# Optimization experiments

Measured on AMD Instinct MI355X. Metric: run time of the kernel, lower is better.

## Reference

```python
import jax, jax.numpy as jnp
import numpy as np

RADIUS = 12
SIGMA = 5.0
USM_LO, USM_HI = 0.0, 5.0
BEGIN = 0  # cfg.usm_begin_param


def _gauss_kernel_2d():
    x = jnp.arange(-RADIUS, RADIUS + 1, dtype=jnp.float32)
    k = jnp.exp(-0.5 * (x / SIGMA) ** 2)
    k = k / k.sum()
    return jnp.outer(k, k)  # [25, 25]


def setup_inputs() -> dict:
    key = jax.random.key(0)
    k1, k2 = jax.random.split(key)
    img = jax.random.uniform(k1, (16, 3, 512, 512), dtype=jnp.float32)
    features = jax.random.normal(k2, (16, 8), dtype=jnp.float32)
    return {"img": img, "features": features}


def reference(img, features):
    p = features[:, BEGIN:BEGIN + 1]                       # [B, 1]
    param = (jnp.tanh(p) * 0.5 + 0.5) * (USM_HI - USM_LO) + USM_LO

    # depthwise 25x25 gaussian blur with reflect padding
    kernel = jnp.broadcast_to(_gauss_kernel_2d(), (3, 1, 25, 25))  # OIHW, groups=3
    padded = jnp.pad(img, ((0, 0), (0, 0), (RADIUS, RADIUS), (RADIUS, RADIUS)),
                     mode='reflect')
    blurred = jax.lax.conv_general_dilated(
        padded, kernel, window_strides=(1, 1), padding='VALID',
        dimension_numbers=('NCHW', 'OIHW', 'NCHW'), feature_group_count=3)

    out = img + param.reshape(-1, 1, 1, 1) * (img - blurred)
    return out, param
```

## Files before the change

### kernel.cpp

```cpp
#include <hip/hip_runtime.h>
#include <hip/hip_fp16.h>


#define RADIUS 12
#define KS     25
#define TILE   64
#define PT     (TILE + 2 * RADIUS)
#define TA_LD  104
#define TB_LD  72
#define IMG_W  512
#define IMG_H  512
#define PLANE  (IMG_W * IMG_H)
#define NPLANE 48

__device__ __constant__ float GW[KS] = {
    0.00453456f, 0.00718308f, 0.01093238f, 0.01598625f, 0.02245983f,
    0.03031760f, 0.03931982f, 0.04899550f, 0.05865827f, 0.06747307f,
    0.07456928f, 0.07918039f, 0.08077993f, 0.07918039f, 0.07456928f,
    0.06747307f, 0.05865827f, 0.04899550f, 0.03931982f, 0.03031760f,
    0.02245983f, 0.01598625f, 0.01093238f, 0.00718308f, 0.00453456f
};

__device__ __forceinline__ int reflect512(int i) {
    i = (i < 0) ? -i : i;
    return (i >= 512) ? (1022 - i) : i;
}

typedef _Float16 h2_t __attribute__((ext_vector_type(2)));

__device__ __forceinline__ unsigned h2u(__half2 h) {
    union { __half2 h; unsigned u; } x; x.h = h; return x.u;
}
__device__ __forceinline__ float u_lo(unsigned u) {
    union { unsigned u; __half2 h; } x; x.u = u;
    return __half2float(__low2half(x.h));
}
__device__ __forceinline__ float u_hi(unsigned u) {
    union { unsigned u; __half2 h; } x; x.u = u;
    return __half2float(__high2half(x.h));
}

#if __has_builtin(__builtin_amdgcn_fdot2)
#define HAVE_DOT2 1
__device__ __forceinline__ float fdot2u(unsigned a, unsigned b, float c) {
    union { unsigned u; h2_t h; } ua, ub;
    ua.u = a; ub.u = b;
    return __builtin_amdgcn_fdot2(ua.h, ub.h, c, false);
}
#else
#define HAVE_DOT2 0
__device__ __forceinline__ float fdot2u(unsigned a, unsigned b, float c) {
    return c + u_lo(a) * u_lo(b) + u_hi(a) * u_hi(b);
}
#endif

__global__ __launch_bounds__(256) void usm_fused_kernel(
    const float* __restrict__ img, const float* __restrict__ feat,
    float* __restrict__ out, float* __restrict__ out_param)
{
    __shared__ __half tileA[PT][TA_LD];
    __shared__ __half tmpB[PT][TB_LD];

    const int tid = threadIdx.x;
    const int tx0 = blockIdx.x * TILE, ty0 = blockIdx.y * TILE;
    const int zc = blockIdx.z, b = zc / 3;
    const float param = (tanhf(feat[b * 8]) * 0.5f + 0.5f) * 5.0f;
    const float* __restrict__ src = img + (size_t)zc * PLANE;
    const bool xedge = (blockIdx.x == 0) || (blockIdx.x == 7);

    unsigned W2[12];
#pragma unroll
    for (int m = 0; m < 12; ++m)
        W2[m] = h2u(__floats2half2_rn(GW[2 * m], GW[2 * m + 1]));
    const unsigned WE = h2u(__floats2half2_rn(GW[24], 0.f));
    const unsigned WO = h2u(__floats2half2_rn(0.f, GW[24]));

    for (int li = tid; li < PT * 11; li += 256) {
        int py = li / 11, s = li - py * 11;
        int gy = reflect512(ty0 - RADIUS + py);
        const float* rowp = src + gy * IMG_W;
        int gx = tx0 - RADIUS + s * 8;
        float4 va, vb;
        if (!xedge) {
            va = *(const float4*)(rowp + gx);
            vb = *(const float4*)(rowp + gx + 4);
        } else {
            va.x = rowp[reflect512(gx)];     va.y = rowp[reflect512(gx + 1)];
            va.z = rowp[reflect512(gx + 2)]; va.w = rowp[reflect512(gx + 3)];
            vb.x = rowp[reflect512(gx + 4)]; vb.y = rowp[reflect512(gx + 5)];
            vb.z = rowp[reflect512(gx + 6)]; vb.w = rowp[reflect512(gx + 7)];
        }
        uint4 pk;
        pk.x = h2u(__floats2half2_rn(va.x, va.y));
        pk.y = h2u(__floats2half2_rn(va.z, va.w));
        pk.z = h2u(__floats2half2_rn(vb.x, vb.y));
        pk.w = h2u(__floats2half2_rn(vb.z, vb.w));
        *(uint4*)&tileA[py][s * 8] = pk;
    }
    __syncthreads();

    for (int li = tid; li < PT * (TILE / 8); li += 256) {
        const int py = li >> 3, g = li & 7;
        const uint4 qa = *(const uint4*)&tileA[py][g * 8];
        const uint4 qb = *(const uint4*)&tileA[py][g * 8 + 8];
        const uint4 qc = *(const uint4*)&tileA[py][g * 8 + 16];
        const uint4 qd = *(const uint4*)&tileA[py][g * 8 + 24];

        unsigned P[16] = { qa.x, qa.y, qa.z, qa.w, qb.x, qb.y, qb.z, qb.w,
                           qc.x, qc.y, qc.z, qc.w, qd.x, qd.y, qd.z, qd.w };
        unsigned S[15];
#pragma unroll
        for (int i = 0; i < 15; ++i)
            S[i] = __builtin_amdgcn_alignbit(P[i + 1], P[i], 16);

        float acc[8];
#pragma unroll
        for (int h = 0; h < 4; ++h) {
            float a = 0.f;
#pragma unroll
            for (int m = 0; m < 12; ++m) a = fdot2u(P[h + m], W2[m], a);
            acc[2 * h] = fdot2u(P[h + 12], WE, a);
        }
#pragma unroll
        for (int h = 0; h < 4; ++h) {
            float a = 0.f;
#pragma unroll
            for (int m = 0; m < 12; ++m) a = fdot2u(S[h + m], W2[m], a);
            acc[2 * h + 1] = fdot2u(P[h + 12], WO, a);
        }

        uint4 pk;
        pk.x = h2u(__floats2half2_rn(acc[0], acc[1]));
        pk.y = h2u(__floats2half2_rn(acc[2], acc[3]));
        pk.z = h2u(__floats2half2_rn(acc[4], acc[5]));
        pk.w = h2u(__floats2half2_rn(acc[6], acc[7]));
        *(uint4*)&tmpB[py][g * 8] = pk;
    }
    __syncthreads();

    const int tx4 = (tid & 15) * 4, ry0 = (tid >> 4) * 4;
    float ax[4], ay[4], az[4], aw[4];
#pragma unroll
    for (int d = 0; d < 4; ++d) ax[d] = ay[d] = az[d] = aw[d] = 0.f;

#pragma unroll
    for (int k = 0; k < KS + 3; ++k) {
        uint2 rd = *(const uint2*)&tmpB[ry0 + k][tx4];
        const float c0 = u_lo(rd.x), c1 = u_hi(rd.x);
        const float c2 = u_lo(rd.y), c3 = u_hi(rd.y);
#pragma unroll
        for (int d = 0; d < 4; ++d) {
            int kk = k - d;
            if (kk >= 0 && kk < KS) {
                const float wk = GW[kk];
                ax[d] += wk * c0; ay[d] += wk * c1;
                az[d] += wk * c2; aw[d] += wk * c3;
            }
        }
    }

    float* __restrict__ dst = out + (size_t)zc * PLANE;
#pragma unroll
    for (int d = 0; d < 4; ++d) {
        const int oy = ty0 + ry0 + d;
        float4 v = *(const float4*)(src + (size_t)oy * IMG_W + tx0 + tx4);
        float4 o;
        o.x = v.x + param * (v.x - ax[d]);
        o.y = v.y + param * (v.y - ay[d]);
        o.z = v.z + param * (v.z - az[d]);
        o.w = v.w + param * (v.w - aw[d]);
        *(float4*)(dst + (size_t)oy * IMG_W + tx0 + tx4) = o;
    }

    if (tid == 0 && blockIdx.x == 0 && blockIdx.y == 0 && (zc - b * 3) == 0)
        out_param[b] = param;
}

extern "C" void kernel_launch(void* const* d_in, const int* in_sizes, int n_in,
                              void* d_out, int out_size, void* d_ws, size_t ws_size,
                              hipStream_t stream) {
    const float* img  = (const float*)d_in[0];
    const float* feat = (const float*)d_in[1];
    float* out       = (float*)d_out;
    float* out_param = (float*)d_out + (size_t)NPLANE * PLANE;

    usm_fused_kernel<<<dim3(8, 8, NPLANE), 256, 0, stream>>>(img, feat, out, out_param);
}
```

Measured before the change: 42.17 us.

## Swizzle block order, unroll staging loops, use fp16 vertical FMA and LDS center

Result: faster. 40.44 us (-4.1%).

```diff
diff --git a/kernel.cpp b/kernel.cpp
--- a/kernel.cpp
+++ b/kernel.cpp
@@ -13,6 +13,9 @@
 #define PLANE  (IMG_W * IMG_H)
 #define NPLANE 48
 
+#define N_STAGE (PT * 11)
+#define N_H     (PT * (TILE / 8))
+
 __device__ __constant__ float GW[KS] = {
     0.00453456f, 0.00718308f, 0.01093238f, 0.01598625f, 0.02245983f,
     0.03031760f, 0.03931982f, 0.04899550f, 0.05865827f, 0.06747307f,
@@ -31,24 +34,23 @@
 __device__ __forceinline__ unsigned h2u(__half2 h) {
     union { __half2 h; unsigned u; } x; x.h = h; return x.u;
 }
+__device__ __forceinline__ __half2 u2h(unsigned u) {
+    union { unsigned u; __half2 h; } x; x.u = u; return x.h;
+}
 __device__ __forceinline__ float u_lo(unsigned u) {
-    union { unsigned u; __half2 h; } x; x.u = u;
-    return __half2float(__low2half(x.h));
+    return __half2float(__low2half(u2h(u)));
 }
 __device__ __forceinline__ float u_hi(unsigned u) {
-    union { unsigned u; __half2 h; } x; x.u = u;
-    return __half2float(__high2half(x.h));
+    return __half2float(__high2half(u2h(u)));
 }
 
 #if __has_builtin(__builtin_amdgcn_fdot2)
-#define HAVE_DOT2 1
 __device__ __forceinline__ float fdot2u(unsigned a, unsigned b, float c) {
     union { unsigned u; h2_t h; } ua, ub;
     ua.u = a; ub.u = b;
     return __builtin_amdgcn_fdot2(ua.h, ub.h, c, false);
 }
 #else
-#define HAVE_DOT2 0
 __device__ __forceinline__ float fdot2u(unsigned a, unsigned b, float c) {
     return c + u_lo(a) * u_lo(b) + u_hi(a) * u_hi(b);
 }
@@ -61,12 +63,18 @@
     __shared__ __half tileA[PT][TA_LD];
     __shared__ __half tmpB[PT][TB_LD];
 
+    const int bid  = blockIdx.x + 8 * blockIdx.y + 64 * blockIdx.z;
+    const int swz  = (bid & 7) * 384 + (bid >> 3);
+    const int bx   = swz & 7;
+    const int by   = (swz >> 3) & 7;
+    const int zc   = swz >> 6;
+
     const int tid = threadIdx.x;
-    const int tx0 = blockIdx.x * TILE, ty0 = blockIdx.y * TILE;
-    const int zc = blockIdx.z, b = zc / 3;
+    const int tx0 = bx * TILE, ty0 = by * TILE;
+    const int b   = zc / 3;
     const float param = (tanhf(feat[b * 8]) * 0.5f + 0.5f) * 5.0f;
     const float* __restrict__ src = img + (size_t)zc * PLANE;
-    const bool xedge = (blockIdx.x == 0) || (blockIdx.x == 7);
+    const bool xedge = (bx == 0) || (bx == 7);
 
     unsigned W2[12];
 #pragma unroll
@@ -75,86 +83,98 @@
     const unsigned WE = h2u(__floats2half2_rn(GW[24], 0.f));
     const unsigned WO = h2u(__floats2half2_rn(0.f, GW[24]));
 
-    for (int li = tid; li < PT * 11; li += 256) {
-        int py = li / 11, s = li - py * 11;
-        int gy = reflect512(ty0 - RADIUS + py);
-        const float* rowp = src + gy * IMG_W;
-        int gx = tx0 - RADIUS + s * 8;
-        float4 va, vb;
-        if (!xedge) {
-            va = *(const float4*)(rowp + gx);
-            vb = *(const float4*)(rowp + gx + 4);
-        } else {
-            va.x = rowp[reflect512(gx)];     va.y = rowp[reflect512(gx + 1)];
-            va.z = rowp[reflect512(gx + 2)]; va.w = rowp[reflect512(gx + 3)];
-            vb.x = rowp[reflect512(gx + 4)]; vb.y = rowp[reflect512(gx + 5)];
-            vb.z = rowp[reflect512(gx + 6)]; vb.w = rowp[reflect512(gx + 7)];
+    __half2 GWh2[KS];
+#pragma unroll
+    for (int k = 0; k < KS; ++k)
+        GWh2[k] = __floats2half2_rn(GW[k], GW[k]);
+
+#pragma unroll
+    for (int it = 0; it < 4; ++it) {
+        const int li = tid + it * 256;
+        if (it < 3 || li < N_STAGE) {
+            const int py = li / 11, s = li - py * 11;
+            const int gy = reflect512(ty0 - RADIUS + py);
+            const float* __restrict__ rowp = src + (size_t)gy * IMG_W;
+            const int gx = tx0 - RADIUS + s * 8;
+            float4 va, vb;
+            if (!xedge) {
+                va = *(const float4*)(rowp + gx);
+                vb = *(const float4*)(rowp + gx + 4);
+            } else {
+                va.x = rowp[reflect512(gx)];     va.y = rowp[reflect512(gx + 1)];
+                va.z = rowp[reflect512(gx + 2)]; va.w = rowp[reflect512(gx + 3)];
+                vb.x = rowp[reflect512(gx + 4)]; vb.y = rowp[reflect512(gx + 5)];
+                vb.z = rowp[reflect512(gx + 6)]; vb.w = rowp[reflect512(gx + 7)];
+            }
+            uint4 pk;
+            pk.x = h2u(__floats2half2_rn(va.x, va.y));
+            pk.y = h2u(__floats2half2_rn(va.z, va.w));
+            pk.z = h2u(__floats2half2_rn(vb.x, vb.y));
+            pk.w = h2u(__floats2half2_rn(vb.z, vb.w));
+            *(uint4*)&tileA[py][s * 8] = pk;
         }
-        uint4 pk;
-        pk.x = h2u(__floats2half2_rn(va.x, va.y));
-        pk.y = h2u(__floats2half2_rn(va.z, va.w));
-        pk.z = h2u(__floats2half2_rn(vb.x, vb.y));
-        pk.w = h2u(__floats2half2_rn(vb.z, vb.w));
-        *(uint4*)&tileA[py][s * 8] = pk;
     }
     __syncthreads();
 
-    for (int li = tid; li < PT * (TILE / 8); li += 256) {
-        const int py = li >> 3, g = li & 7;
-        const uint4 qa = *(const uint4*)&tileA[py][g * 8];
-        const uint4 qb = *(const uint4*)&tileA[py][g * 8 + 8];
-        const uint4 qc = *(const uint4*)&tileA[py][g * 8 + 16];
-        const uint4 qd = *(const uint4*)&tileA[py][g * 8 + 24];
-
-        unsigned P[16] = { qa.x, qa.y, qa.z, qa.w, qb.x, qb.y, qb.z, qb.w,
-                           qc.x, qc.y, qc.z, qc.w, qd.x, qd.y, qd.z, qd.w };
-        unsigned S[15];
-#pragma unroll
-        for (int i = 0; i < 15; ++i)
-            S[i] = __builtin_amdgcn_alignbit(P[i + 1], P[i], 16);
-
-        float acc[8];
-#pragma unroll
-        for (int h = 0; h < 4; ++h) {
-            float a = 0.f;
-#pragma unroll
-            for (int m = 0; m < 12; ++m) a = fdot2u(P[h + m], W2[m], a);
-            acc[2 * h] = fdot2u(P[h + 12], WE, a);
+#pragma unroll
+    for (int it = 0; it < 3; ++it) {
+        const int li = tid + it * 256;
+        if (it < 2 || li < N_H) {
+            const int py = li >> 3, g = li & 7;
+            const uint4 qa = *(const uint4*)&tileA[py][g * 8];
+            const uint4 qb = *(const uint4*)&tileA[py][g * 8 + 8];
+            const uint4 qc = *(const uint4*)&tileA[py][g * 8 + 16];
+            const uint4 qd = *(const uint4*)&tileA[py][g * 8 + 24];
+
+            unsigned P[16] = { qa.x, qa.y, qa.z, qa.w, qb.x, qb.y, qb.z, qb.w,
+                               qc.x, qc.y, qc.z, qc.w, qd.x, qd.y, qd.z, qd.w };
+            unsigned S[15];
+#pragma unroll
+            for (int i = 0; i < 15; ++i)
+                S[i] = __builtin_amdgcn_alignbit(P[i + 1], P[i], 16);
+
+            float acc[8];
+#pragma unroll
+            for (int h = 0; h < 4; ++h) {
+                float a = 0.f;
+#pragma unroll
+                for (int m = 0; m < 12; ++m) a = fdot2u(P[h + m], W2[m], a);
+                acc[2 * h] = fdot2u(P[h + 12], WE, a);
+            }
+#pragma unroll
+            for (int h = 0; h < 4; ++h) {
+                float a = 0.f;
+#pragma unroll
+                for (int m = 0; m < 12; ++m) a = fdot2u(S[h + m], W2[m], a);
+                acc[2 * h + 1] = fdot2u(P[h + 12], WO, a);
+            }
+
+            uint4 pk;
+            pk.x = h2u(__floats2half2_rn(acc[0], acc[1]));
+            pk.y = h2u(__floats2half2_rn(acc[2], acc[3]));
+            pk.z = h2u(__floats2half2_rn(acc[4], acc[5]));
+            pk.w = h2u(__floats2half2_rn(acc[6], acc[7]));
+            *(uint4*)&tmpB[py][g * 8] = pk;
         }
-#pragma unroll
-        for (int h = 0; h < 4; ++h) {
-            float a = 0.f;
-#pragma unroll
-            for (int m = 0; m < 12; ++m) a = fdot2u(S[h + m], W2[m], a);
-            acc[2 * h + 1] = fdot2u(P[h + 12], WO, a);
-        }
-
-        uint4 pk;
-        pk.x = h2u(__floats2half2_rn(acc[0], acc[1]));
-        pk.y = h2u(__floats2half2_rn(acc[2], acc[3]));
-        pk.z = h2u(__floats2half2_rn(acc[4], acc[5]));
-        pk.w = h2u(__floats2half2_rn(acc[6], acc[7]));
-        *(uint4*)&tmpB[py][g * 8] = pk;
     }
     __syncthreads();
 
     const int tx4 = (tid & 15) * 4, ry0 = (tid >> 4) * 4;
-    float ax[4], ay[4], az[4], aw[4];
-#pragma unroll
-    for (int d = 0; d < 4; ++d) ax[d] = ay[d] = az[d] = aw[d] = 0.f;
+
+    __half2 aP0[4], aP1[4];
+#pragma unroll
+    for (int d = 0; d < 4; ++d) { aP0[d] = __half2(0, 0); aP1[d] = __half2(0, 0); }
 
 #pragma unroll
     for (int k = 0; k < KS + 3; ++k) {
-        uint2 rd = *(const uint2*)&tmpB[ry0 + k][tx4];
-        const float c0 = u_lo(rd.x), c1 = u_hi(rd.x);
-        const float c2 = u_lo(rd.y), c3 = u_hi(rd.y);
+        const uint2 rd = *(const uint2*)&tmpB[ry0 + k][tx4];
+        const __half2 p0 = u2h(rd.x), p1 = u2h(rd.y);
 #pragma unroll
         for (int d = 0; d < 4; ++d) {
-            int kk = k - d;
+            const int kk = k - d;
             if (kk >= 0 && kk < KS) {
-                const float wk = GW[kk];
-                ax[d] += wk * c0; ay[d] += wk * c1;
-                az[d] += wk * c2; aw[d] += wk * c3;
+                aP0[d] = __hfma2(GWh2[kk], p0, aP0[d]);
+                aP1[d] = __hfma2(GWh2[kk], p1, aP1[d]);
             }
         }
     }
@@ -163,16 +183,19 @@
 #pragma unroll
     for (int d = 0; d < 4; ++d) {
         const int oy = ty0 + ry0 + d;
-        float4 v = *(const float4*)(src + (size_t)oy * IMG_W + tx0 + tx4);
+        const uint2 cv = *(const uint2*)&tileA[ry0 + d + RADIUS][tx4 + RADIUS];
+        const float v0 = u_lo(cv.x), v1 = u_hi(cv.x), v2 = u_lo(cv.y), v3 = u_hi(cv.y);
+        const float b0 = __half2float(__low2half(aP0[d])), b1 = __half2float(__high2half(aP0[d]));
+        const float b2 = __half2float(__low2half(aP1[d])), b3 = __half2float(__high2half(aP1[d]));
         float4 o;
-        o.x = v.x + param * (v.x - ax[d]);
-        o.y = v.y + param * (v.y - ay[d]);
-        o.z = v.z + param * (v.z - az[d]);
-        o.w = v.w + param * (v.w - aw[d]);
+        o.x = v0 + param * (v0 - b0);
+        o.y = v1 + param * (v1 - b1);
+        o.z = v2 + param * (v2 - b2);
+        o.w = v3 + param * (v3 - b3);
         *(float4*)(dst + (size_t)oy * IMG_W + tx0 + tx4) = o;
     }
 
-    if (tid == 0 && blockIdx.x == 0 && blockIdx.y == 0 && (zc - b * 3) == 0)
+    if (tid == 0 && bx == 0 && by == 0 && (zc - b * 3) == 0)
         out_param[b] = param;
 }
 
```
